# Optimization experiments

Measured on AMD Instinct MI355X. Metric: run time of the kernel, lower is better.

Reference implementation:

```python
import jax, jax.numpy as jnp
import numpy as np

N = 100000      # nodes
E = 1600000     # edges
F_IN = 64       # node_features
F_OUT = 32      # output_size


def _cheb2(H, row, col, w_norm, theta, bias):
    # ChebConv K=2, sym normalization, lambda_max=2 (GCLSTM default):
    # L_hat = L - I = -D^{-1/2} A D^{-1/2}, so T0 = H, T1 = -A_norm H
    agg = jax.ops.segment_sum(w_norm[:, None] * H[col], row, num_segments=N)  # [N, F_OUT]
    return H @ theta[0] - agg @ theta[1] + bias


def setup_inputs() -> dict:
    key = jax.random.key(0)
    ks = jax.random.split(key, 24)
    inp = {}
    inp["x"] = jax.random.normal(ks[0], (N, F_IN), jnp.float32)
    inp["edge_index"] = jax.random.randint(ks[1], (2, E), 0, N)
    inp["edge_weight"] = jax.random.uniform(ks[2], (E,), jnp.float32)
    inp["h"] = jax.random.normal(ks[3], (N, F_OUT), jnp.float32)
    inp["c"] = jax.random.normal(ks[4], (N, F_OUT), jnp.float32)
    s_in = float(1.0 / np.sqrt(F_IN))
    s_out = float(1.0 / np.sqrt(F_OUT))
    i = 5
    for g in "ifco":
        inp[f"W_{g}"] = jax.random.uniform(ks[i], (F_IN, F_OUT), jnp.float32, -s_in, s_in); i += 1
        inp[f"b_{g}"] = jax.random.uniform(ks[i], (1, F_OUT), jnp.float32, -s_in, s_in); i += 1
        inp[f"theta_{g}"] = jax.random.uniform(ks[i], (2, F_OUT, F_OUT), jnp.float32, -s_out, s_out); i += 1
        inp[f"cb_{g}"] = jax.random.uniform(ks[i], (F_OUT,), jnp.float32, -s_out, s_out); i += 1
    inp["W_lin"] = jax.random.uniform(ks[i], (F_OUT, 1), jnp.float32, -s_out, s_out); i += 1
    inp["b_lin"] = jax.random.uniform(ks[i], (1,), jnp.float32, -s_out, s_out)
    return inp


def reference(x, edge_index, edge_weight, h, c,
              W_i, b_i, theta_i, cb_i,
              W_f, b_f, theta_f, cb_f,
              W_c, b_c, theta_c, cb_c,
              W_o, b_o, theta_o, cb_o,
              W_lin, b_lin):
    row, col = edge_index[0], edge_index[1]
    # symmetric normalization of edge weights (get_laplacian 'sym')
    deg = jax.ops.segment_sum(edge_weight, row, num_segments=N)
    dis = jnp.where(deg > 0, jax.lax.rsqrt(jnp.where(deg > 0, deg, 1.0)), 0.0)
    w_norm = dis[row] * edge_weight * dis[col]  # [E]
    # GCLSTM gates: input x through dense W, hidden h through ChebConv
    I = jax.nn.sigmoid(x @ W_i + _cheb2(h, row, col, w_norm, theta_i, cb_i) + b_i)
    Fg = jax.nn.sigmoid(x @ W_f + _cheb2(h, row, col, w_norm, theta_f, cb_f) + b_f)
    T = jnp.tanh(x @ W_c + _cheb2(h, row, col, w_norm, theta_c, cb_c) + b_c)
    C = Fg * c + I * T
    O = jax.nn.sigmoid(x @ W_o + _cheb2(h, row, col, w_norm, theta_o, cb_o) + b_o)
    H = O * jnp.tanh(C)
    # wrapper head: relu then Linear(out, 1)
    return jax.nn.relu(H) @ W_lin + b_lin  # [N, 1]
```

## Files before the change

kernel.cpp:

```cpp
#include <hip/hip_runtime.h>
#include <math.h>

#define NN 100000
#define NE 1600000
#define EPB 8192
#define NEB 196
#define NBUK 391
#define CAP 8192

#define DEGSCALE 16777216.0f

typedef __attribute__((ext_vector_type(8))) short bf16x8;
typedef __attribute__((ext_vector_type(4))) float f32x4;

#define MFMA(A, B, C) __builtin_amdgcn_mfma_f32_16x16x32_bf16(A, B, C, 0, 0, 0)

__device__ __forceinline__ float sigm(float z) { return 1.0f / (1.0f + expf(-z)); }

__device__ __forceinline__ void split1(float v, unsigned short* hi, unsigned short* lo) {
  unsigned u = __float_as_uint(v);
  *hi = (unsigned short)(u >> 16);
  float hf = __uint_as_float(u & 0xFFFF0000u);
  float lf = v - hf;
  *lo = (unsigned short)(__float_as_uint(lf) >> 16);
}

__device__ __forceinline__ void split8(const float* f, bf16x8* hi, bf16x8* lo) {
#pragma unroll
  for (int j = 0; j < 8; ++j) {
    unsigned short h, l;
    split1(f[j], &h, &l);
    (*hi)[j] = (short)h;
    (*lo)[j] = (short)l;
  }
}

__device__ __forceinline__ bf16x8 as_bf16x8(uint4 q) {
  union { uint4 q; bf16x8 v; } u;
  u.q = q;
  return u.v;
}

__device__ __forceinline__ void load8(const float4* p, int idx4, float* f) {
  float4 a = p[idx4];
  float4 b = p[idx4 + 1];
  f[0] = a.x; f[1] = a.y; f[2] = a.z; f[3] = a.w;
  f[4] = b.x; f[5] = b.y; f[6] = b.z; f[7] = b.w;
}


__global__ __launch_bounds__(256) void k_p1(const int* __restrict__ row,
                                            int* __restrict__ counts) {
  __shared__ int hist[NBUK];
  for (int i = threadIdx.x; i < NBUK; i += 256) hist[i] = 0;
  __syncthreads();
  int e0 = blockIdx.x * EPB;
  int e1 = min(e0 + EPB, NE);
  for (int e = e0 + (int)threadIdx.x; e < e1; e += 256)
    atomicAdd(&hist[row[e] >> 8], 1);
  __syncthreads();
  for (int i = threadIdx.x; i < NBUK; i += 256)
    counts[blockIdx.x * NBUK + i] = hist[i];
}

__global__ __launch_bounds__(256) void k_s1(int* __restrict__ counts,
                                            int* __restrict__ total) {
  __shared__ int s[256];
  int b = blockIdx.x;
  int t = threadIdx.x;
  int v = (t < NEB) ? counts[t * NBUK + b] : 0;
  s[t] = v;
  __syncthreads();
  for (int o = 1; o < 256; o <<= 1) {
    int a = (t >= o) ? s[t - o] : 0;
    __syncthreads();
    s[t] += a;
    __syncthreads();
  }
  if (t < NEB) counts[t * NBUK + b] = s[t] - v;
  if (t == 255) total[b] = s[255];
}

__global__ __launch_bounds__(512) void k_s2(const int* __restrict__ total,
                                            int* __restrict__ bases) {
  __shared__ int s[512];
  int t = threadIdx.x;
  int v = (t < NBUK) ? total[t] : 0;
  s[t] = v;
  __syncthreads();
  for (int o = 1; o < 512; o <<= 1) {
    int a = (t >= o) ? s[t - o] : 0;
    __syncthreads();
    s[t] += a;
    __syncthreads();
  }
  if (t < NBUK) bases[t] = s[t] - v;
  if (t == 0) bases[NBUK] = NE;
}

__global__ __launch_bounds__(256) void k_p2(const int* __restrict__ row,
                                            const int* __restrict__ col,
                                            const float* __restrict__ ew,
                                            const int* __restrict__ rel,
                                            const int* __restrict__ bases,
                                            int2* __restrict__ colw) {
  __shared__ int cursor[NBUK];
  for (int i = threadIdx.x; i < NBUK; i += 256)
    cursor[i] = bases[i] + rel[blockIdx.x * NBUK + i];
  __syncthreads();
  int e0 = blockIdx.x * EPB;
  int e1 = min(e0 + EPB, NE);
  for (int e = e0 + (int)threadIdx.x; e < e1; e += 256) {
    int r = row[e];
    int c = col[e];
    float w = ew[e];
    int slot = atomicAdd(&cursor[r >> 8], 1);
    colw[slot] = make_int2(c | ((r & 255) << 17), __float_as_int(w));
  }
}

__global__ __launch_bounds__(256) void k_bucket(const int* __restrict__ bases,
                                               int2* __restrict__ colw,
                                               int* __restrict__ rowptr,
                                               float* __restrict__ dis) {
  __shared__ int2 stage[CAP];
  __shared__ int cnt[256], degfx[256], s[256], cursor[256];
  int b = blockIdx.x;
  int base = bases[b];
  int M = bases[b + 1] - base;
  if (M > CAP) M = CAP;
  int t = threadIdx.x;
  cnt[t] = 0;
  degfx[t] = 0;
  __syncthreads();
  for (int i = t; i < M; i += 256) {
    int2 e = colw[base + i];
    stage[i] = e;
    int rl = (e.x >> 17) & 255;
    atomicAdd(&cnt[rl], 1);
    unsigned fx = (unsigned)(__int_as_float(e.y) * DEGSCALE + 0.5f);
    atomicAdd((unsigned*)&degfx[rl], fx);
  }
  __syncthreads();
  int v = cnt[t];
  s[t] = v;
  __syncthreads();
  for (int o = 1; o < 256; o <<= 1) {
    int a = (t >= o) ? s[t - o] : 0;
    __syncthreads();
    s[t] += a;
    __syncthreads();
  }
  int excl = s[t] - v;
  int node = b * 256 + t;
  if (node <= NN) rowptr[node] = base + excl;
  if (node < NN) {
    unsigned fx = (unsigned)degfx[t];
    dis[node] = fx ? rsqrtf((float)fx * (1.0f / DEGSCALE)) : 0.0f;
  }
  cursor[t] = excl;
  __syncthreads();
  for (int i = t; i < M; i += 256) {
    int2 e = stage[i];
    int rl = (e.x >> 17) & 255;
    int r = atomicAdd(&cursor[rl], 1);
    colw[base + r] = e;
  }
}

__global__ __launch_bounds__(256) void k_agg(const int* __restrict__ rowptr,
                                             const int2* __restrict__ colw,
                                             const float* __restrict__ dis,
                                             const float4* __restrict__ h4,
                                             float4* __restrict__ agg4) {
  int n = (blockIdx.x * 256 + threadIdx.x) >> 6;
  if (n >= NN) return;
  int lane = threadIdx.x & 63;
  int es = lane >> 3;
  int fg = lane & 7;
  int s0 = rowptr[n];
  int s1 = rowptr[n + 1];
  float4 a0 = make_float4(0.f, 0.f, 0.f, 0.f);
  float4 a1 = a0;
  int j = s0 + es;
  for (; j + 8 < s1; j += 16) {
    int2 cw0 = colw[j];
    int2 cw1 = colw[j + 8];
    int c0 = cw0.x & 0x1FFFF;
    int c1 = cw1.x & 0x1FFFF;
    float w0 = __int_as_float(cw0.y) * dis[c0];
    float w1 = __int_as_float(cw1.y) * dis[c1];
    float4 h0 = h4[c0 * 8 + fg];
    float4 h1 = h4[c1 * 8 + fg];
    a0.x = fmaf(w0, h0.x, a0.x); a0.y = fmaf(w0, h0.y, a0.y);
    a0.z = fmaf(w0, h0.z, a0.z); a0.w = fmaf(w0, h0.w, a0.w);
    a1.x = fmaf(w1, h1.x, a1.x); a1.y = fmaf(w1, h1.y, a1.y);
    a1.z = fmaf(w1, h1.z, a1.z); a1.w = fmaf(w1, h1.w, a1.w);
  }
  if (j < s1) {
    int2 cw0 = colw[j];
    int c0 = cw0.x & 0x1FFFF;
    float w0 = __int_as_float(cw0.y) * dis[c0];
    float4 h0 = h4[c0 * 8 + fg];
    a0.x = fmaf(w0, h0.x, a0.x); a0.y = fmaf(w0, h0.y, a0.y);
    a0.z = fmaf(w0, h0.z, a0.z); a0.w = fmaf(w0, h0.w, a0.w);
  }
  a0.x += a1.x; a0.y += a1.y; a0.z += a1.z; a0.w += a1.w;
#pragma unroll
  for (int o = 8; o < 64; o <<= 1) {
    a0.x += __shfl_xor(a0.x, o, 64);
    a0.y += __shfl_xor(a0.y, o, 64);
    a0.z += __shfl_xor(a0.z, o, 64);
    a0.w += __shfl_xor(a0.w, o, 64);
  }
  if (es == 0) {
    float dn = dis[n];
    a0.x *= dn; a0.y *= dn; a0.z *= dn; a0.w *= dn;
    agg4[n * 8 + fg] = a0;
  }
}

struct PrepParams {
  const float* W[4];
  const float* T0[4];
  const float* T1[4];
  const float* b[4];
  const float* cb[4];
  uint4* fh;
  uint4* fl;
  float* bias;
};

__global__ __launch_bounds__(256) void k_prep(PrepParams pp) {
  int idx = blockIdx.x * 256 + threadIdx.x;
  if (idx < 2048) {
    int T = idx >> 6;
    int lane = idx & 63;
    int ncol = ((T & 7) * 16) + (lane & 15);
    int g = ncol >> 5;
    int c = ncol & 31;
    int kq = (lane >> 4) * 8;
    const float* mat;
    int kbase;
    if (T < 16) { mat = pp.W[g]; kbase = (T >> 3) * 32 + kq; }
    else if (T < 24) { mat = pp.T0[g]; kbase = kq; }
    else { mat = pp.T1[g]; kbase = kq; }
    unsigned hw[4], lw[4];
#pragma unroll
    for (int jj = 0; jj < 4; ++jj) {
      unsigned short h0, l0, h1, l1;
      split1(mat[(kbase + 2 * jj) * 32 + c], &h0, &l0);
      split1(mat[(kbase + 2 * jj + 1) * 32 + c], &h1, &l1);
      hw[jj] = (unsigned)h0 | ((unsigned)h1 << 16);
      lw[jj] = (unsigned)l0 | ((unsigned)l1 << 16);
    }
    pp.fh[idx] = make_uint4(hw[0], hw[1], hw[2], hw[3]);
    pp.fl[idx] = make_uint4(lw[0], lw[1], lw[2], lw[3]);
  }
  if (blockIdx.x == 0 && threadIdx.x < 128) {
    int g = threadIdx.x >> 5;
    int c = threadIdx.x & 31;
    pp.bias[threadIdx.x] = pp.b[g][c] + pp.cb[g][c];
  }
}

struct GmmParams {
  const float4* x4;
  const float4* h4;
  const float4* agg4;
  const float* cst;
  const uint4* fh;
  const uint4* fl;
  const float* bias;
  const float* wlin;
  const float* blin;
  float* out;
};

__global__ __launch_bounds__(256) void k_gmm(GmmParams p) {
  const int lane = threadIdx.x & 63;
  const int wv = threadIdx.x >> 6;
  const int m0 = blockIdx.x * 64 + wv * 16;
  const int mr = lane & 15;
  const int quad = lane >> 4;
  int m = m0 + mr;
  if (m >= NN) m = NN - 1;

  bf16x8 xh[2], xl[2], hh, hl, gh, gl;
  float f[8];
#pragma unroll
  for (int kt = 0; kt < 2; ++kt) {
    load8(p.x4, (m * 64 + kt * 32 + quad * 8) >> 2, f);
    split8(f, &xh[kt], &xl[kt]);
  }
  load8(p.h4, (m * 32 + quad * 8) >> 2, f);
  split8(f, &hh, &hl);
  load8(p.agg4, (m * 32 + quad * 8) >> 2, f);
#pragma unroll
  for (int j = 0; j < 8; ++j) f[j] = -f[j];
  split8(f, &gh, &gl);

  float wl0 = p.wlin[mr];
  float wl1 = p.wlin[mr + 16];
  float bl = p.blin[0];

  f32x4 acc[8];
#pragma unroll 2
  for (int nt = 0; nt < 8; ++nt) {
    float bv = p.bias[nt * 16 + mr];
    f32x4 a;
    a[0] = bv; a[1] = bv; a[2] = bv; a[3] = bv;
    bf16x8 b0h = as_bf16x8(p.fh[nt * 64 + lane]);
    bf16x8 b0l = as_bf16x8(p.fl[nt * 64 + lane]);
    bf16x8 b1h = as_bf16x8(p.fh[(8 + nt) * 64 + lane]);
    bf16x8 b1l = as_bf16x8(p.fl[(8 + nt) * 64 + lane]);
    bf16x8 t0h = as_bf16x8(p.fh[(16 + nt) * 64 + lane]);
    bf16x8 t0l = as_bf16x8(p.fl[(16 + nt) * 64 + lane]);
    bf16x8 t1h = as_bf16x8(p.fh[(24 + nt) * 64 + lane]);
    bf16x8 t1l = as_bf16x8(p.fl[(24 + nt) * 64 + lane]);
    a = MFMA(xh[0], b0h, a); a = MFMA(xh[0], b0l, a); a = MFMA(xl[0], b0h, a);
    a = MFMA(xh[1], b1h, a); a = MFMA(xh[1], b1l, a); a = MFMA(xl[1], b1h, a);
    a = MFMA(hh, t0h, a);    a = MFMA(hh, t0l, a);    a = MFMA(hl, t0h, a);
    a = MFMA(gh, t1h, a);    a = MFMA(gh, t1l, a);    a = MFMA(gl, t1h, a);
    acc[nt] = a;
  }

#pragma unroll
  for (int r = 0; r < 4; ++r) {
    int node = m0 + quad * 4 + r;
    int nc = node < NN ? node : NN - 1;
    float c0 = p.cst[nc * 32 + mr];
    float c1 = p.cst[nc * 32 + 16 + mr];
    float I0 = sigm(acc[0][r]), I1 = sigm(acc[1][r]);
    float F0 = sigm(acc[2][r]), F1 = sigm(acc[3][r]);
    float T0 = tanhf(acc[4][r]), T1 = tanhf(acc[5][r]);
    float O0 = sigm(acc[6][r]), O1 = sigm(acc[7][r]);
    float C0 = fmaf(F0, c0, I0 * T0);
    float C1 = fmaf(F1, c1, I1 * T1);
    float H0 = O0 * tanhf(C0);
    float H1 = O1 * tanhf(C1);
    float part = fmaf(fmaxf(H0, 0.f), wl0, fmaxf(H1, 0.f) * wl1);
#pragma unroll
    for (int s = 1; s < 16; s <<= 1) part += __shfl_xor(part, s, 64);
    if (mr == 0 && node < NN) p.out[node] = part + bl;
  }
}

extern "C" void kernel_launch(void* const* d_in, const int* in_sizes, int n_in,
                              void* d_out, int out_size, void* d_ws, size_t ws_size,
                              hipStream_t stream) {
  const float* x = (const float*)d_in[0];
  const int* row = (const int*)d_in[1];
  const int* col = row + NE;
  const float* ew = (const float*)d_in[2];
  const float* h = (const float*)d_in[3];
  const float* c = (const float*)d_in[4];

  float* ws = (float*)d_ws;
  float* dis = ws;
  int* rowptr = (int*)(ws + 100000);
  int* counts = (int*)(ws + 200004);
  int* total = (int*)(ws + 276640);
  int* bases = (int*)(ws + 277032);
  uint4* fh = (uint4*)(ws + 277424);
  uint4* fl = (uint4*)(ws + 285616);
  float* biasws = ws + 293808;
  int2* colw = (int2*)(ws + 293936);
  float* agg = ws + 293936 + 2 * NE;

  k_p1<<<NEB, 256, 0, stream>>>(row, counts);
  k_s1<<<NBUK, 256, 0, stream>>>(counts, total);
  k_s2<<<1, 512, 0, stream>>>(total, bases);
  k_p2<<<NEB, 256, 0, stream>>>(row, col, ew, counts, bases, colw);
  k_bucket<<<NBUK, 256, 0, stream>>>(bases, colw, rowptr, dis);

  PrepParams pp;
  for (int g = 0; g < 4; ++g) {
    pp.W[g] = (const float*)d_in[5 + 4 * g];
    pp.b[g] = (const float*)d_in[6 + 4 * g];
    pp.T0[g] = (const float*)d_in[7 + 4 * g];
    pp.T1[g] = pp.T0[g] + 1024;
    pp.cb[g] = (const float*)d_in[8 + 4 * g];
  }
  pp.fh = fh;
  pp.fl = fl;
  pp.bias = biasws;
  k_prep<<<8, 256, 0, stream>>>(pp);

  k_agg<<<(NN + 3) / 4, 256, 0, stream>>>(rowptr, colw, dis, (const float4*)h,
                                          (float4*)agg);

  GmmParams gp;
  gp.x4 = (const float4*)x;
  gp.h4 = (const float4*)h;
  gp.agg4 = (const float4*)agg;
  gp.cst = c;
  gp.fh = fh;
  gp.fl = fl;
  gp.bias = biasws;
  gp.wlin = (const float*)d_in[21];
  gp.blin = (const float*)d_in[22];
  gp.out = (float*)d_out;
  k_gmm<<<(NN + 63) / 64, 256, 0, stream>>>(gp);
}
```

Baseline: 256.3 us.

## Fuse neighbor aggregation into gate GEMM kernel and merge prep with scan

The separate aggregation kernel is removed. Each lane of the gate GEMM kernel now gathers its node's neighbours directly, covering the 8 features it needs, and builds the negated normalized aggregate in registers. This drops the agg buffer write and re-read. The weight-splitting prep kernel is also merged into the bucket-base scan kernel, saving a launch. The trade-off is that the gather loses its parallelism: 4 lanes per node walk all edges serially instead of 64 lanes splitting the edges, so latency per wave may grow and load balance may suffer.

Measured after the change: 250.8 us. -2.2%, faster.

```diff
diff --git a/kernel.cpp b/kernel.cpp
--- a/kernel.cpp
+++ b/kernel.cpp
@@ -81,21 +81,66 @@
   if (t == 255) total[b] = s[255];
 }
 
-__global__ __launch_bounds__(512) void k_s2(const int* __restrict__ total,
-                                            int* __restrict__ bases) {
-  __shared__ int s[512];
-  int t = threadIdx.x;
-  int v = (t < NBUK) ? total[t] : 0;
-  s[t] = v;
-  __syncthreads();
-  for (int o = 1; o < 512; o <<= 1) {
-    int a = (t >= o) ? s[t - o] : 0;
-    __syncthreads();
-    s[t] += a;
-    __syncthreads();
-  }
-  if (t < NBUK) bases[t] = s[t] - v;
-  if (t == 0) bases[NBUK] = NE;
+struct S2PParams {
+  const int* total;
+  int* bases;
+  const float* W[4];
+  const float* T0[4];
+  const float* T1[4];
+  const float* b[4];
+  const float* cb[4];
+  uint4* fh;
+  uint4* fl;
+  float* bias;
+};
+
+__global__ __launch_bounds__(512) void k_s2p(S2PParams pp) {
+  if (blockIdx.x == 0) {
+    __shared__ int s[512];
+    int t = threadIdx.x;
+    int v = (t < NBUK) ? pp.total[t] : 0;
+    s[t] = v;
+    __syncthreads();
+    for (int o = 1; o < 512; o <<= 1) {
+      int a = (t >= o) ? s[t - o] : 0;
+      __syncthreads();
+      s[t] += a;
+      __syncthreads();
+    }
+    if (t < NBUK) pp.bases[t] = s[t] - v;
+    if (t == 0) pp.bases[NBUK] = NE;
+    return;
+  }
+  int idx = (blockIdx.x - 1) * 512 + threadIdx.x;
+  if (idx < 2048) {
+    int T = idx >> 6;
+    int lane = idx & 63;
+    int ncol = ((T & 7) * 16) + (lane & 15);
+    int g = ncol >> 5;
+    int c = ncol & 31;
+    int kq = (lane >> 4) * 8;
+    const float* mat;
+    int kbase;
+    if (T < 16) { mat = pp.W[g]; kbase = (T >> 3) * 32 + kq; }
+    else if (T < 24) { mat = pp.T0[g]; kbase = kq; }
+    else { mat = pp.T1[g]; kbase = kq; }
+    unsigned hw[4], lw[4];
+#pragma unroll
+    for (int jj = 0; jj < 4; ++jj) {
+      unsigned short h0, l0, h1, l1;
+      split1(mat[(kbase + 2 * jj) * 32 + c], &h0, &l0);
+      split1(mat[(kbase + 2 * jj + 1) * 32 + c], &h1, &l1);
+      hw[jj] = (unsigned)h0 | ((unsigned)h1 << 16);
+      lw[jj] = (unsigned)l0 | ((unsigned)l1 << 16);
+    }
+    pp.fh[idx] = make_uint4(hw[0], hw[1], hw[2], hw[3]);
+    pp.fl[idx] = make_uint4(lw[0], lw[1], lw[2], lw[3]);
+  }
+  if (blockIdx.x == 1 && threadIdx.x < 128) {
+    int g = threadIdx.x >> 5;
+    int c = threadIdx.x & 31;
+    pp.bias[threadIdx.x] = pp.b[g][c] + pp.cb[g][c];
+  }
 }
 
 __global__ __launch_bounds__(256) void k_p2(const int* __restrict__ row,
@@ -168,107 +213,13 @@
   }
 }
 
-__global__ __launch_bounds__(256) void k_agg(const int* __restrict__ rowptr,
-                                             const int2* __restrict__ colw,
-                                             const float* __restrict__ dis,
-                                             const float4* __restrict__ h4,
-                                             float4* __restrict__ agg4) {
-  int n = (blockIdx.x * 256 + threadIdx.x) >> 6;
-  if (n >= NN) return;
-  int lane = threadIdx.x & 63;
-  int es = lane >> 3;
-  int fg = lane & 7;
-  int s0 = rowptr[n];
-  int s1 = rowptr[n + 1];
-  float4 a0 = make_float4(0.f, 0.f, 0.f, 0.f);
-  float4 a1 = a0;
-  int j = s0 + es;
-  for (; j + 8 < s1; j += 16) {
-    int2 cw0 = colw[j];
-    int2 cw1 = colw[j + 8];
-    int c0 = cw0.x & 0x1FFFF;
-    int c1 = cw1.x & 0x1FFFF;
-    float w0 = __int_as_float(cw0.y) * dis[c0];
-    float w1 = __int_as_float(cw1.y) * dis[c1];
-    float4 h0 = h4[c0 * 8 + fg];
-    float4 h1 = h4[c1 * 8 + fg];
-    a0.x = fmaf(w0, h0.x, a0.x); a0.y = fmaf(w0, h0.y, a0.y);
-    a0.z = fmaf(w0, h0.z, a0.z); a0.w = fmaf(w0, h0.w, a0.w);
-    a1.x = fmaf(w1, h1.x, a1.x); a1.y = fmaf(w1, h1.y, a1.y);
-    a1.z = fmaf(w1, h1.z, a1.z); a1.w = fmaf(w1, h1.w, a1.w);
-  }
-  if (j < s1) {
-    int2 cw0 = colw[j];
-    int c0 = cw0.x & 0x1FFFF;
-    float w0 = __int_as_float(cw0.y) * dis[c0];
-    float4 h0 = h4[c0 * 8 + fg];
-    a0.x = fmaf(w0, h0.x, a0.x); a0.y = fmaf(w0, h0.y, a0.y);
-    a0.z = fmaf(w0, h0.z, a0.z); a0.w = fmaf(w0, h0.w, a0.w);
-  }
-  a0.x += a1.x; a0.y += a1.y; a0.z += a1.z; a0.w += a1.w;
-#pragma unroll
-  for (int o = 8; o < 64; o <<= 1) {
-    a0.x += __shfl_xor(a0.x, o, 64);
-    a0.y += __shfl_xor(a0.y, o, 64);
-    a0.z += __shfl_xor(a0.z, o, 64);
-    a0.w += __shfl_xor(a0.w, o, 64);
-  }
-  if (es == 0) {
-    float dn = dis[n];
-    a0.x *= dn; a0.y *= dn; a0.z *= dn; a0.w *= dn;
-    agg4[n * 8 + fg] = a0;
-  }
-}
-
-struct PrepParams {
-  const float* W[4];
-  const float* T0[4];
-  const float* T1[4];
-  const float* b[4];
-  const float* cb[4];
-  uint4* fh;
-  uint4* fl;
-  float* bias;
-};
-
-__global__ __launch_bounds__(256) void k_prep(PrepParams pp) {
-  int idx = blockIdx.x * 256 + threadIdx.x;
-  if (idx < 2048) {
-    int T = idx >> 6;
-    int lane = idx & 63;
-    int ncol = ((T & 7) * 16) + (lane & 15);
-    int g = ncol >> 5;
-    int c = ncol & 31;
-    int kq = (lane >> 4) * 8;
-    const float* mat;
-    int kbase;
-    if (T < 16) { mat = pp.W[g]; kbase = (T >> 3) * 32 + kq; }
-    else if (T < 24) { mat = pp.T0[g]; kbase = kq; }
-    else { mat = pp.T1[g]; kbase = kq; }
-    unsigned hw[4], lw[4];
-#pragma unroll
-    for (int jj = 0; jj < 4; ++jj) {
-      unsigned short h0, l0, h1, l1;
-      split1(mat[(kbase + 2 * jj) * 32 + c], &h0, &l0);
-      split1(mat[(kbase + 2 * jj + 1) * 32 + c], &h1, &l1);
-      hw[jj] = (unsigned)h0 | ((unsigned)h1 << 16);
-      lw[jj] = (unsigned)l0 | ((unsigned)l1 << 16);
-    }
-    pp.fh[idx] = make_uint4(hw[0], hw[1], hw[2], hw[3]);
-    pp.fl[idx] = make_uint4(lw[0], lw[1], lw[2], lw[3]);
-  }
-  if (blockIdx.x == 0 && threadIdx.x < 128) {
-    int g = threadIdx.x >> 5;
-    int c = threadIdx.x & 31;
-    pp.bias[threadIdx.x] = pp.b[g][c] + pp.cb[g][c];
-  }
-}
-
-struct GmmParams {
+struct FusedParams {
   const float4* x4;
   const float4* h4;
-  const float4* agg4;
   const float* cst;
+  const int* rowptr;
+  const int2* colw;
+  const float* dis;
   const uint4* fh;
   const uint4* fl;
   const float* bias;
@@ -277,7 +228,7 @@
   float* out;
 };
 
-__global__ __launch_bounds__(256) void k_gmm(GmmParams p) {
+__global__ __launch_bounds__(256) void k_fused(FusedParams p) {
   const int lane = threadIdx.x & 63;
   const int wv = threadIdx.x >> 6;
   const int m0 = blockIdx.x * 64 + wv * 16;
@@ -295,10 +246,51 @@
   }
   load8(p.h4, (m * 32 + quad * 8) >> 2, f);
   split8(f, &hh, &hl);
-  load8(p.agg4, (m * 32 + quad * 8) >> 2, f);
-#pragma unroll
-  for (int j = 0; j < 8; ++j) f[j] = -f[j];
-  split8(f, &gh, &gl);
+
+  float fa[8] = {0.f, 0.f, 0.f, 0.f, 0.f, 0.f, 0.f, 0.f};
+  float fb[8] = {0.f, 0.f, 0.f, 0.f, 0.f, 0.f, 0.f, 0.f};
+  {
+    int s0 = p.rowptr[m];
+    int s1v = p.rowptr[m + 1];
+    int j = s0;
+    for (; j + 1 < s1v; j += 2) {
+      int2 cw0 = p.colw[j];
+      int2 cw1 = p.colw[j + 1];
+      int c0 = cw0.x & 0x1FFFF;
+      int c1 = cw1.x & 0x1FFFF;
+      float w0 = __int_as_float(cw0.y) * p.dis[c0];
+      float w1 = __int_as_float(cw1.y) * p.dis[c1];
+      const float4* hp0 = p.h4 + c0 * 8 + quad * 2;
+      const float4* hp1 = p.h4 + c1 * 8 + quad * 2;
+      float4 a0 = hp0[0], a1 = hp0[1];
+      float4 b0 = hp1[0], b1 = hp1[1];
+      fa[0] = fmaf(w0, a0.x, fa[0]); fa[1] = fmaf(w0, a0.y, fa[1]);
+      fa[2] = fmaf(w0, a0.z, fa[2]); fa[3] = fmaf(w0, a0.w, fa[3]);
+      fa[4] = fmaf(w0, a1.x, fa[4]); fa[5] = fmaf(w0, a1.y, fa[5]);
+      fa[6] = fmaf(w0, a1.z, fa[6]); fa[7] = fmaf(w0, a1.w, fa[7]);
+      fb[0] = fmaf(w1, b0.x, fb[0]); fb[1] = fmaf(w1, b0.y, fb[1]);
+      fb[2] = fmaf(w1, b0.z, fb[2]); fb[3] = fmaf(w1, b0.w, fb[3]);
+      fb[4] = fmaf(w1, b1.x, fb[4]); fb[5] = fmaf(w1, b1.y, fb[5]);
+      fb[6] = fmaf(w1, b1.z, fb[6]); fb[7] = fmaf(w1, b1.w, fb[7]);
+    }
+    if (j < s1v) {
+      int2 cw0 = p.colw[j];
+      int c0 = cw0.x & 0x1FFFF;
+      float w0 = __int_as_float(cw0.y) * p.dis[c0];
+      const float4* hp0 = p.h4 + c0 * 8 + quad * 2;
+      float4 a0 = hp0[0], a1 = hp0[1];
+      fa[0] = fmaf(w0, a0.x, fa[0]); fa[1] = fmaf(w0, a0.y, fa[1]);
+      fa[2] = fmaf(w0, a0.z, fa[2]); fa[3] = fmaf(w0, a0.w, fa[3]);
+      fa[4] = fmaf(w0, a1.x, fa[4]); fa[5] = fmaf(w0, a1.y, fa[5]);
+      fa[6] = fmaf(w0, a1.z, fa[6]); fa[7] = fmaf(w0, a1.w, fa[7]);
+    }
+  }
+  {
+    float dn = -p.dis[m];
+#pragma unroll
+    for (int j = 0; j < 8; ++j) f[j] = dn * (fa[j] + fb[j]);
+    split8(f, &gh, &gl);
+  }
 
   float wl0 = p.wlin[mr];
   float wl1 = p.wlin[mr + 16];
@@ -366,40 +358,40 @@
   uint4* fl = (uint4*)(ws + 285616);
   float* biasws = ws + 293808;
   int2* colw = (int2*)(ws + 293936);
-  float* agg = ws + 293936 + 2 * NE;
 
   k_p1<<<NEB, 256, 0, stream>>>(row, counts);
   k_s1<<<NBUK, 256, 0, stream>>>(counts, total);
-  k_s2<<<1, 512, 0, stream>>>(total, bases);
+
+  S2PParams sp;
+  sp.total = total;
+  sp.bases = bases;
+  for (int g = 0; g < 4; ++g) {
+    sp.W[g] = (const float*)d_in[5 + 4 * g];
+    sp.b[g] = (const float*)d_in[6 + 4 * g];
+    sp.T0[g] = (const float*)d_in[7 + 4 * g];
+    sp.T1[g] = sp.T0[g] + 1024;
+    sp.cb[g] = (const float*)d_in[8 + 4 * g];
+  }
+  sp.fh = fh;
+  sp.fl = fl;
+  sp.bias = biasws;
+  k_s2p<<<9, 512, 0, stream>>>(sp);
+
   k_p2<<<NEB, 256, 0, stream>>>(row, col, ew, counts, bases, colw);
   k_bucket<<<NBUK, 256, 0, stream>>>(bases, colw, rowptr, dis);
 
-  PrepParams pp;
-  for (int g = 0; g < 4; ++g) {
-    pp.W[g] = (const float*)d_in[5 + 4 * g];
-    pp.b[g] = (const float*)d_in[6 + 4 * g];
-    pp.T0[g] = (const float*)d_in[7 + 4 * g];
-    pp.T1[g] = pp.T0[g] + 1024;
-    pp.cb[g] = (const float*)d_in[8 + 4 * g];
-  }
-  pp.fh = fh;
-  pp.fl = fl;
-  pp.bias = biasws;
-  k_prep<<<8, 256, 0, stream>>>(pp);
-
-  k_agg<<<(NN + 3) / 4, 256, 0, stream>>>(rowptr, colw, dis, (const float4*)h,
-                                          (float4*)agg);
-
-  GmmParams gp;
-  gp.x4 = (const float4*)x;
-  gp.h4 = (const float4*)h;
-  gp.agg4 = (const float4*)agg;
-  gp.cst = c;
-  gp.fh = fh;
-  gp.fl = fl;
-  gp.bias = biasws;
-  gp.wlin = (const float*)d_in[21];
-  gp.blin = (const float*)d_in[22];
-  gp.out = (float*)d_out;
-  k_gmm<<<(NN + 63) / 64, 256, 0, stream>>>(gp);
-}
+  FusedParams fp;
+  fp.x4 = (const float4*)x;
+  fp.h4 = (const float4*)h;
+  fp.cst = c;
+  fp.rowptr = rowptr;
+  fp.colw = colw;
+  fp.dis = dis;
+  fp.fh = fh;
+  fp.fl = fl;
+  fp.bias = biasws;
+  fp.wlin = (const float*)d_in[21];
+  fp.blin = (const float*)d_in[22];
+  fp.out = (float*)d_out;
+  k_fused<<<(NN + 63) / 64, 256, 0, stream>>>(fp);
+}
```
